# Kernel optimization log

Hardware: AMD Instinct MI355X
Metric: run time of the kernel (lower is better)

Reference implementation:

```python
import jax, jax.numpy as jnp
import numpy as np

E = 250000   # n_scanned_edges
B = 16       # batch_size
N = 50000    # n_entities (n_nodes)
R = 500      # n_relations
D_IN = 100   # input embedding dim (proj input)
D = 64       # n_dims_sm
M = 2 * E    # n_memorized_and_scanned_nodes (>= n_vi_groups + n_vj_groups)


def setup_inputs() -> dict:
    rng = np.random.default_rng(0)
    eg = rng.integers(0, B, E)
    vi = rng.integers(0, N, E)
    vj = rng.integers(0, N, E)
    order = np.lexsort((vj, vi, eg))  # sorted by (eg_idx, vi, vj) as the module assumes
    eg, vi, vj = eg[order], vi[order], vj[order]
    rel = rng.integers(0, R, E)
    # dense group ids; idx_vi is non-decreasing because edges are lexsorted by (eg,vi)
    idx_vi = np.unique(eg.astype(np.int64) * N + vi, return_inverse=True)[1]
    idx_vj = np.unique(eg.astype(np.int64) * N + vj, return_inverse=True)[1]
    n_vi = int(idx_vi.max()) + 1
    edges = np.stack([eg, vi, vj, rel, idx_vi, idx_vj, idx_vi, n_vi + idx_vj], 1).astype(np.int32)

    key = jax.random.key(0)
    ks = jax.random.split(key, 24)
    nrm = lambda k, shp, s=1.0: jax.random.normal(k, shp, jnp.float32) * s
    na = jax.random.uniform(ks[0], (B, N), jnp.float32)
    na = na / jnp.sum(na, 1, keepdims=True)  # node attention is a distribution per example
    inp = {
        "node_attention": na,
        "scanned_edges": jnp.asarray(edges),
        "hidden_uncon": nrm(ks[1], (1, N, D_IN)),
        "hidden_con": nrm(ks[2], (M, D_IN)),
        "rel_table": nrm(ks[3], (R, D_IN)),
        "query_head_emb": nrm(ks[4], (B, D_IN)),
        "query_rel_emb": nrm(ks[5], (B, D_IN)),
        "p_W": nrm(ks[6], (D_IN, D), 0.1),
        "p_b": jnp.zeros((D,), jnp.float32),
    }
    i = 7
    for g in ("g1", "g2"):
        for nm, shp in (("lW", (4 * D, D)), ("lb", (D,)), ("rW", (4 * D, D)), ("rb", (D,)), ("cW", (D, D)), ("cb", (D,))):
            inp[g + "_" + nm] = nrm(ks[i], shp, 0.05)
            i += 1
    return inp


def _g(left, right, lW, lb, rW, rb, cW, cb):
    # G layer: sum(left_dense(cat(left)) * center_dense(right_dense(cat(right))), -1)
    lx = jnp.concatenate(left, -1)
    rx = jnp.concatenate(right, -1)
    l = jax.nn.leaky_relu(lx @ lW + lb, 0.2)  # tf.nn.leaky_relu alpha=0.2
    r = jax.nn.leaky_relu(rx @ rW + rb, 0.2)
    return jnp.sum(l * (r @ cW + cb), -1)


def reference(node_attention, scanned_edges, hidden_uncon, hidden_con, rel_table,
              query_head_emb, query_rel_emb, p_W, p_b,
              g1_lW, g1_lb, g1_rW, g1_rb, g1_cW, g1_cb,
              g2_lW, g2_lb, g2_rW, g2_rb, g2_cW, g2_cb):
    Bn, Nn = node_attention.shape
    En = scanned_edges.shape[0]
    proj = lambda x: jnp.tanh(x @ p_W + p_b)

    h_con = proj(hidden_con)       # (M, D)
    h_uncon = proj(hidden_uncon)   # (1, N, D)
    qh = proj(query_head_emb)      # (B, D)
    qr = proj(query_rel_emb)

    e = scanned_edges
    eg, vi, vj = e[:, 0], e[:, 1], e[:, 2]
    idx_vi = e[:, 4]
    # node2edge gathers
    h_vi = h_con[e[:, 6]]          # (E, D)
    h_vj = h_con[e[:, 7]]
    hu_vj = h_uncon[0][vj]         # hidden_uncon batch is 1 -> idx 0
    remb = proj(rel_table[e[:, 3]])
    qhv = qh[eg]
    qrv = qr[eg]

    left = (h_vi, remb, qhv, qrv)
    logits = _g(left, (h_vj, remb, qhv, qrv), g1_lW, g1_lb, g1_rW, g1_rb, g1_cW, g1_cb)
    logits = logits + _g(left, (hu_vj, remb, qhv, qrv), g2_lW, g2_lb, g2_rW, g2_rb, g2_cW, g2_cb)

    # neighbor softmax over sorted idx_vi segments
    m = jax.ops.segment_max(logits, idx_vi, num_segments=En, indices_are_sorted=True)
    ex = jnp.exp(logits - m[idx_vi])
    den = jax.ops.segment_sum(ex, idx_vi, num_segments=En, indices_are_sorted=True)
    transition = ex / den[idx_vi]

    # flow attention: gather at (eg, vi), scatter-sum at (eg, vj)
    trans_att = node_attention[eg, vi] * transition
    new_att = jnp.zeros((Bn, Nn), node_attention.dtype).at[eg, vj].add(trans_att)
    new_att = new_att / jnp.sum(new_att, axis=1, keepdims=True)
    return new_att
```

## Files before the change

### kernel.cpp

```cpp
#include <hip/hip_runtime.h>

#define DIN 100
#define DD  64
#define NE  250000
#define NB  16
#define NN  50000
#define NR  500
#define NM  500000
#define NH  (NM + NN)

#define H_OFF    64
#define TA2_OFF  (H_OFF + NH*DD)
#define RT_OFF   (TA2_OFF + NE*DD)
#define QT_OFF   (RT_OFF + 4*NR*DD)
#define LG_OFF   (QT_OFF + 4*NB*DD)

#define PA 320
#define PB 160
#define PC 32

#define XT_STRIDE 260

__device__ __forceinline__ void fma4x4(const float4 x, const float4 w, float4 acc[4]) {
  acc[0].x += x.x*w.x; acc[0].y += x.x*w.y; acc[0].z += x.x*w.z; acc[0].w += x.x*w.w;
  acc[1].x += x.y*w.x; acc[1].y += x.y*w.y; acc[1].z += x.y*w.z; acc[1].w += x.y*w.w;
  acc[2].x += x.z*w.x; acc[2].y += x.z*w.y; acc[2].z += x.z*w.z; acc[2].w += x.z*w.w;
  acc[3].x += x.w*w.x; acc[3].y += x.w*w.y; acc[3].z += x.w*w.z; acc[3].w += x.w*w.w;
}

__device__ __forceinline__ float4 leaky4(float4 v) {
  v.x = v.x > 0.f ? v.x : 0.2f*v.x;
  v.y = v.y > 0.f ? v.y : 0.2f*v.y;
  v.z = v.z > 0.f ? v.z : 0.2f*v.z;
  v.w = v.w > 0.f ? v.w : 0.2f*v.w;
  return v;
}

__global__ void k_init(int* wsI, float* bsum) {
  if (threadIdx.x == 0) { wsI[0] = 0x7fffffff; wsI[1] = 0; }
  if (threadIdx.x < NB) bsum[threadIdx.x] = 0.f;
}

__global__ void k_limits(const int* __restrict__ edges, int* __restrict__ wsI) {
  int i = blockIdx.x * blockDim.x + threadIdx.x;
  int mn = 0x7fffffff, mx = -1;
  if (i < NE) { int v = edges[i*8 + 7]; mn = v; mx = v; }
  for (int off = 32; off > 0; off >>= 1) {
    mn = min(mn, __shfl_down(mn, off));
    mx = max(mx, __shfl_down(mx, off));
  }
  if ((threadIdx.x & 63) == 0) {
    atomicMin(&wsI[0], mn);
    atomicMax(&wsI[1], mx + 1);
  }
}

__global__ void k_tables(const float* __restrict__ rtab,
                         const float* __restrict__ qh, const float* __restrict__ qr,
                         const float* __restrict__ pW, const float* __restrict__ pb,
                         const float* __restrict__ g1_lW, const float* __restrict__ g1_lb,
                         const float* __restrict__ g1_rW, const float* __restrict__ g1_rb,
                         const float* __restrict__ g2_lW, const float* __restrict__ g2_lb,
                         const float* __restrict__ g2_rW, const float* __restrict__ g2_rb,
                         float* __restrict__ rT, float* __restrict__ qT) {
  __shared__ float xs[DIN], xs2[DIN], ps[DD], ps2[DD];
  const int d = threadIdx.x;
  const int blk = blockIdx.x;
  if (blk < NR) {
    for (int k = d; k < DIN; k += 64) xs[k] = rtab[blk*DIN + k];
    __syncthreads();
    float a = pb[d];
    for (int k = 0; k < DIN; ++k) a += xs[k] * pW[k*DD + d];
    ps[d] = tanhf(a);
    __syncthreads();
    float o1 = 0.f, o2 = 0.f, o3 = 0.f, o4 = 0.f;
    for (int k = 0; k < DD; ++k) {
      float p = ps[k];
      o1 += p * g1_lW[(DD + k)*DD + d];
      o2 += p * g1_rW[(DD + k)*DD + d];
      o3 += p * g2_lW[(DD + k)*DD + d];
      o4 += p * g2_rW[(DD + k)*DD + d];
    }
    rT[(0*NR + blk)*DD + d] = o1;
    rT[(1*NR + blk)*DD + d] = o2;
    rT[(2*NR + blk)*DD + d] = o3;
    rT[(3*NR + blk)*DD + d] = o4;
  } else {
    const int b = blk - NR;
    for (int k = d; k < DIN; k += 64) { xs[k] = qh[b*DIN + k]; xs2[k] = qr[b*DIN + k]; }
    __syncthreads();
    float a = pb[d], a2 = pb[d];
    for (int k = 0; k < DIN; ++k) { a += xs[k]*pW[k*DD + d]; a2 += xs2[k]*pW[k*DD + d]; }
    ps[d] = tanhf(a); ps2[d] = tanhf(a2);
    __syncthreads();
    float o1 = g1_lb[d], o2 = g1_rb[d], o3 = g2_lb[d], o4 = g2_rb[d];
    for (int k = 0; k < DD; ++k) {
      float p = ps[k], p2 = ps2[k];
      o1 += p * g1_lW[(2*DD + k)*DD + d] + p2 * g1_lW[(3*DD + k)*DD + d];
      o2 += p * g1_rW[(2*DD + k)*DD + d] + p2 * g1_rW[(3*DD + k)*DD + d];
      o3 += p * g2_lW[(2*DD + k)*DD + d] + p2 * g2_lW[(3*DD + k)*DD + d];
      o4 += p * g2_rW[(2*DD + k)*DD + d] + p2 * g2_rW[(3*DD + k)*DD + d];
    }
    qT[(0*NB + b)*DD + d] = o1;
    qT[(1*NB + b)*DD + d] = o2;
    qT[(2*NB + b)*DD + d] = o3;
    qT[(3*NB + b)*DD + d] = o4;
  }
}

__global__ __launch_bounds__(256, 2)
void k_proj(const float* __restrict__ hcon, const float* __restrict__ huncon,
            const float* __restrict__ pW, const float* __restrict__ pb,
            const int* __restrict__ lim, float* __restrict__ H) {
  __shared__ __align__(16) float pWs[DIN*DD];
  __shared__ __align__(16) float Xt[52][XT_STRIDE];
  const int tid = threadIdx.x;
  for (int i = tid; i < DIN*DD; i += 256) pWs[i] = pW[i];
  const int tc = tid & 7, tr = tid >> 3;
  const int c0 = tc << 3;
  const float4 pb0 = *(const float4*)&pb[c0];
  const float4 pb1 = *(const float4*)&pb[c0 + 4];
  const int nmax = lim[1];
  const int t_lo = (nmax + 255) >> 8;
  const int NT   = t_lo + ((NN + 255) >> 8);
  __syncthreads();
  for (int t = blockIdx.x; t < NT; t += gridDim.x) {
    const int row0 = (t < t_lo) ? (t << 8) : (NM + ((t - t_lo) << 8));
    const int myrow = row0 + tid;
    const float* src = nullptr;
    if (myrow < NH) src = (myrow < NM) ? &hcon[myrow*DIN] : &huncon[(myrow - NM)*DIN];
    float4 acc[2][2][4];
    #pragma unroll
    for (int a = 0; a < 2; ++a)
      #pragma unroll
      for (int b = 0; b < 2; ++b)
        #pragma unroll
        for (int i = 0; i < 4; ++i) acc[a][b][i] = make_float4(0.f,0.f,0.f,0.f);
    #pragma unroll
    for (int chunk = 0; chunk < 2; ++chunk) {
      const int kb = chunk ? 48 : 0;
      const int klen = chunk ? 52 : 48;
      __syncthreads();
      if (src) {
        for (int j = 0; j < klen; j += 4) {
          float4 v = *(const float4*)&src[kb + j];
          Xt[j+0][tid] = v.x; Xt[j+1][tid] = v.y; Xt[j+2][tid] = v.z; Xt[j+3][tid] = v.w;
        }
      }
      __syncthreads();
      for (int k = 0; k < klen; ++k) {
        float4 x0 = *(const float4*)&Xt[k][tr*8];
        float4 x1 = *(const float4*)&Xt[k][tr*8 + 4];
        float4 w0 = *(const float4*)&pWs[(kb + k)*DD + c0];
        float4 w1 = *(const float4*)&pWs[(kb + k)*DD + c0 + 4];
        fma4x4(x0, w0, acc[0][0]); fma4x4(x0, w1, acc[0][1]);
        fma4x4(x1, w0, acc[1][0]); fma4x4(x1, w1, acc[1][1]);
      }
    }
    #pragma unroll
    for (int a = 0; a < 2; ++a)
      #pragma unroll
      for (int i = 0; i < 4; ++i) {
        int row = row0 + tr*8 + a*4 + i;
        if (row < NH) {
          float4 o0, o1;
          o0.x = tanhf(acc[a][0][i].x + pb0.x);
          o0.y = tanhf(acc[a][0][i].y + pb0.y);
          o0.z = tanhf(acc[a][0][i].z + pb0.z);
          o0.w = tanhf(acc[a][0][i].w + pb0.w);
          o1.x = tanhf(acc[a][1][i].x + pb1.x);
          o1.y = tanhf(acc[a][1][i].y + pb1.y);
          o1.z = tanhf(acc[a][1][i].z + pb1.z);
          o1.w = tanhf(acc[a][1][i].w + pb1.w);
          *(float4*)&H[row*DD + c0]     = o0;
          *(float4*)&H[row*DD + c0 + 4] = o1;
        }
      }
  }
}

__global__ __launch_bounds__(256, 2)
void k_tf(const float* __restrict__ g1_lW, const float* __restrict__ g1_rW,
          const float* __restrict__ g2_lW, const float* __restrict__ g2_rW,
          const int* __restrict__ lim,
          float* __restrict__ H, float* __restrict__ TA2) {
  __shared__ __align__(16) float Ws0[DD*DD];
  __shared__ __align__(16) float Ws1[DD*DD];
  __shared__ __align__(16) float Ht[32][XT_STRIDE];
  const int tid = threadIdx.x;
  const int nvi  = lim[0];
  const int nmax = lim[1];
  int pool, pbase, pgrid;
  if (blockIdx.x < PA)           { pool = 0; pbase = blockIdx.x;           pgrid = PA; }
  else if (blockIdx.x < PA + PB) { pool = 1; pbase = blockIdx.x - PA;      pgrid = PB; }
  else                           { pool = 2; pbase = blockIdx.x - PA - PB; pgrid = PC; }
  if (pool == 0) {
    for (int i = tid; i < DD*DD; i += 256) { Ws0[i] = g1_lW[i]; Ws1[i] = g2_lW[i]; }
  } else if (pool == 1) {
    for (int i = tid; i < DD*DD; i += 256) Ws0[i] = g1_rW[i];
  } else {
    for (int i = tid; i < DD*DD; i += 256) Ws0[i] = g2_rW[i];
  }
  int t_begin, t_count, row_base;
  if (pool == 0)      { t_begin = 0;        t_count = (nvi + 255) >> 8;                 row_base = 0;  }
  else if (pool == 1) { t_begin = nvi >> 8; t_count = ((nmax + 255) >> 8) - (nvi >> 8); row_base = 0;  }
  else                { t_begin = 0;        t_count = (NN + 255) >> 8;                  row_base = NM; }
  const int tc = tid & 7, tr = tid >> 3;
  const int c0 = tc << 3;
  __syncthreads();
  for (int tt = pbase; tt < t_count; tt += pgrid) {
    const int row0 = row_base + ((t_begin + tt) << 8);
    const int myrow = row0 + tid;
    float4 a0[2][2][4], a1[2][2][4];
    #pragma unroll
    for (int a = 0; a < 2; ++a)
      #pragma unroll
      for (int b = 0; b < 2; ++b)
        #pragma unroll
        for (int i = 0; i < 4; ++i) {
          a0[a][b][i] = make_float4(0.f,0.f,0.f,0.f);
          a1[a][b][i] = make_float4(0.f,0.f,0.f,0.f);
        }
    #pragma unroll
    for (int chunk = 0; chunk < 2; ++chunk) {
      const int kb = chunk << 5;
      __syncthreads();
      if (myrow < NH) {
        const float* src = &H[myrow*DD + kb];
        #pragma unroll
        for (int j = 0; j < 32; j += 4) {
          float4 v = *(const float4*)&src[j];
          Ht[j+0][tid] = v.x; Ht[j+1][tid] = v.y; Ht[j+2][tid] = v.z; Ht[j+3][tid] = v.w;
        }
      }
      __syncthreads();
      if (pool == 0) {
        for (int k = 0; k < 32; ++k) {
          float4 x0 = *(const float4*)&Ht[k][tr*8];
          float4 x1 = *(const float4*)&Ht[k][tr*8 + 4];
          float4 w0 = *(const float4*)&Ws0[(kb + k)*DD + c0];
          float4 w1 = *(const float4*)&Ws0[(kb + k)*DD + c0 + 4];
          float4 u0 = *(const float4*)&Ws1[(kb + k)*DD + c0];
          float4 u1 = *(const float4*)&Ws1[(kb + k)*DD + c0 + 4];
          fma4x4(x0, w0, a0[0][0]); fma4x4(x0, w1, a0[0][1]);
          fma4x4(x1, w0, a0[1][0]); fma4x4(x1, w1, a0[1][1]);
          fma4x4(x0, u0, a1[0][0]); fma4x4(x0, u1, a1[0][1]);
          fma4x4(x1, u0, a1[1][0]); fma4x4(x1, u1, a1[1][1]);
        }
      } else {
        for (int k = 0; k < 32; ++k) {
          float4 x0 = *(const float4*)&Ht[k][tr*8];
          float4 x1 = *(const float4*)&Ht[k][tr*8 + 4];
          float4 w0 = *(const float4*)&Ws0[(kb + k)*DD + c0];
          float4 w1 = *(const float4*)&Ws0[(kb + k)*DD + c0 + 4];
          fma4x4(x0, w0, a0[0][0]); fma4x4(x0, w1, a0[0][1]);
          fma4x4(x1, w0, a0[1][0]); fma4x4(x1, w1, a0[1][1]);
        }
      }
    }
    #pragma unroll
    for (int a = 0; a < 2; ++a)
      #pragma unroll
      for (int i = 0; i < 4; ++i) {
        int row = row0 + tr*8 + a*4 + i;
        bool ok;
        if (pool == 0)      ok = (row < nvi);
        else if (pool == 1) ok = (row >= nvi && row < nmax);
        else                ok = (row < NH);
        if (ok) {
          *(float4*)&H[row*DD + c0]     = a0[a][0][i];
          *(float4*)&H[row*DD + c0 + 4] = a0[a][1][i];
          if (pool == 0) {
            *(float4*)&TA2[row*DD + c0]     = a1[a][0][i];
            *(float4*)&TA2[row*DD + c0 + 4] = a1[a][1][i];
          }
        }
      }
  }
}

__global__ __launch_bounds__(256, 2)
void k_edges(const int* __restrict__ edges,
             const float* __restrict__ TA, const float* __restrict__ TA2,
             const float* __restrict__ HU2,
             const float* __restrict__ rT, const float* __restrict__ qT,
             const float* __restrict__ cW1, const float* __restrict__ cb1,
             const float* __restrict__ cW2, const float* __restrict__ cb2,
             float* __restrict__ logits) {
  __shared__ __align__(16) float Wt1s[DD*68];
  __shared__ __align__(16) float Wt2s[DD*68];
  __shared__ __align__(16) float Lt[DD][68];
  __shared__ __align__(16) float Rt[DD][68];
  __shared__ __align__(16) float4 cbs4[2][16];
  __shared__ float lg[64];
  __shared__ int   se[64*8];
  const int tid = threadIdx.x;
  for (int i = tid; i < DD*DD; i += 256) {
    int k = i >> 6, d = i & 63;
    Wt1s[d*68 + k] = cW1[i];
    Wt2s[d*68 + k] = cW2[i];
  }
  if (tid < 16) {
    cbs4[0][tid] = *(const float4*)&cb1[tid*4];
    cbs4[1][tid] = *(const float4*)&cb2[tid*4];
  }
  const int e   = tid >> 2;
  const int d0  = (tid & 3) * 16;
  const int ee0 = (tid & 15) << 2;
  const int k0  = (tid >> 4) << 2;
  __syncthreads();
  const int NT = (NE + 63) / 64;
  for (int tile = blockIdx.x; tile < NT; tile += gridDim.x) {
    const int e0 = tile * 64;
    const int ecnt = min(64, NE - e0);
    for (int i = tid; i < 64*8; i += 256) se[i] = (i < ecnt*8) ? edges[e0*8 + i] : 0;
    if (tid < 64) lg[tid] = 0.f;
    __syncthreads();
    const int rel = se[e*8 + 3];
    const int eg  = se[e*8 + 0];
    const int li  = se[e*8 + 6];
    for (int g = 0; g < 2; ++g) {
      const float* Lb = g ? TA2 : TA;
      const float* Rb = g ? HU2 : TA;
      const float* rL = rT + (g ? 2*NR*DD : 0);
      const float* rR = rT + (g ? 3*NR*DD : 1*NR*DD);
      const float* qL = qT + (g ? 2*NB*DD : 0);
      const float* qR = qT + (g ? 3*NB*DD : 1*NB*DD);
      const float* Wts = g ? Wt2s : Wt1s;
      const int ri = g ? se[e*8 + 2] : se[e*8 + 7];
      float cbp = 0.f;
      #pragma unroll
      for (int di = 0; di < 4; ++di) {
        const int d = d0 + 4*di;
        float4 l = *(const float4*)&Lb[li*DD + d];
        float4 t = *(const float4*)&rL[rel*DD + d];
        float4 u = *(const float4*)&qL[eg*DD + d];
        l.x += t.x + u.x; l.y += t.y + u.y; l.z += t.z + u.z; l.w += t.w + u.w;
        l = leaky4(l);
        Lt[d+0][e] = l.x; Lt[d+1][e] = l.y; Lt[d+2][e] = l.z; Lt[d+3][e] = l.w;
        float4 c = cbs4[g][d >> 2];
        cbp += l.x*c.x + l.y*c.y + l.z*c.z + l.w*c.w;
        float4 r = *(const float4*)&Rb[ri*DD + d];
        t = *(const float4*)&rR[rel*DD + d];
        u = *(const float4*)&qR[eg*DD + d];
        r.x += t.x + u.x; r.y += t.y + u.y; r.z += t.z + u.z; r.w += t.w + u.w;
        r = leaky4(r);
        Rt[d+0][e] = r.x; Rt[d+1][e] = r.y; Rt[d+2][e] = r.z; Rt[d+3][e] = r.w;
      }
      atomicAdd(&lg[e], cbp);
      __syncthreads();
      float4 z[4] = {{0,0,0,0},{0,0,0,0},{0,0,0,0},{0,0,0,0}};
      for (int d = 0; d < DD; ++d) {
        float4 x = *(const float4*)&Lt[d][ee0];
        float4 w = *(const float4*)&Wts[d*68 + k0];
        fma4x4(x, w, z);
      }
      {
        float4 r0v = *(const float4*)&Rt[k0+0][ee0];
        float4 r1v = *(const float4*)&Rt[k0+1][ee0];
        float4 r2v = *(const float4*)&Rt[k0+2][ee0];
        float4 r3v = *(const float4*)&Rt[k0+3][ee0];
        float p0 = z[0].x*r0v.x + z[0].y*r1v.x + z[0].z*r2v.x + z[0].w*r3v.x;
        float p1 = z[1].x*r0v.y + z[1].y*r1v.y + z[1].z*r2v.y + z[1].w*r3v.y;
        float p2 = z[2].x*r0v.z + z[2].y*r1v.z + z[2].z*r2v.z + z[2].w*r3v.z;
        float p3 = z[3].x*r0v.w + z[3].y*r1v.w + z[3].z*r2v.w + z[3].w*r3v.w;
        atomicAdd(&lg[ee0+0], p0);
        atomicAdd(&lg[ee0+1], p1);
        atomicAdd(&lg[ee0+2], p2);
        atomicAdd(&lg[ee0+3], p3);
      }
      __syncthreads();
    }
    if (tid < ecnt) logits[e0 + tid] = lg[tid];
    __syncthreads();
  }
}

__global__ void k_softmax(const int* __restrict__ edges, const float* __restrict__ logits,
                          const float* __restrict__ na, float* __restrict__ out) {
  int e = blockIdx.x * blockDim.x + threadIdx.x;
  if (e >= NE) return;
  int seg = edges[e*8 + 4];
  if (e > 0 && edges[(e-1)*8 + 4] == seg) return;
  int j = e;
  float m = -1e30f;
  while (j < NE && edges[j*8 + 4] == seg) { m = fmaxf(m, logits[j]); ++j; }
  float s = 0.f;
  for (int t = e; t < j; ++t) s += expf(logits[t] - m);
  int eg = edges[e*8 + 0], vi = edges[e*8 + 1];
  float scale = na[eg*NN + vi] / s;
  for (int t = e; t < j; ++t) {
    int vj = edges[t*8 + 2];
    __hip_atomic_fetch_add(&out[eg*NN + vj], expf(logits[t] - m) * scale,
                           __ATOMIC_RELAXED, __HIP_MEMORY_SCOPE_AGENT);
  }
}

__global__ void k_rowsum(const float* __restrict__ out, float* __restrict__ bsum) {
  int b = blockIdx.y;
  float s = 0.f;
  for (int n = blockIdx.x * blockDim.x + threadIdx.x; n < NN; n += gridDim.x * blockDim.x)
    s += out[b*NN + n];
  for (int off = 32; off > 0; off >>= 1) s += __shfl_down(s, off);
  if ((threadIdx.x & 63) == 0)
    __hip_atomic_fetch_add(&bsum[b], s, __ATOMIC_RELAXED, __HIP_MEMORY_SCOPE_AGENT);
}

__global__ void k_div(float* __restrict__ out, const float* __restrict__ bsum) {
  int i = blockIdx.x * blockDim.x + threadIdx.x;
  if (i < NB*NN) out[i] /= bsum[i / NN];
}

extern "C" void kernel_launch(void* const* d_in, const int* in_sizes, int n_in,
                              void* d_out, int out_size, void* d_ws, size_t ws_size,
                              hipStream_t stream) {
  (void)in_sizes; (void)n_in; (void)out_size; (void)ws_size;
  const float* na     = (const float*)d_in[0];
  const int*   edges  = (const int*)  d_in[1];
  const float* huncon = (const float*)d_in[2];
  const float* hcon   = (const float*)d_in[3];
  const float* rtab   = (const float*)d_in[4];
  const float* qh     = (const float*)d_in[5];
  const float* qr     = (const float*)d_in[6];
  const float* pW     = (const float*)d_in[7];
  const float* pb     = (const float*)d_in[8];
  const float* g1_lW  = (const float*)d_in[9];
  const float* g1_lb  = (const float*)d_in[10];
  const float* g1_rW  = (const float*)d_in[11];
  const float* g1_rb  = (const float*)d_in[12];
  const float* g1_cW  = (const float*)d_in[13];
  const float* g1_cb  = (const float*)d_in[14];
  const float* g2_lW  = (const float*)d_in[15];
  const float* g2_lb  = (const float*)d_in[16];
  const float* g2_rW  = (const float*)d_in[17];
  const float* g2_rb  = (const float*)d_in[18];
  const float* g2_cW  = (const float*)d_in[19];
  const float* g2_cb  = (const float*)d_in[20];
  float* out  = (float*)d_out;
  float* ws   = (float*)d_ws;
  int*   wsI  = (int*)d_ws;
  float* bsum = ws + 16;
  float* H    = ws + H_OFF;
  float* TA2  = ws + TA2_OFF;
  float* rT   = ws + RT_OFF;
  float* qT   = ws + QT_OFF;
  float* lgp  = ws + LG_OFF;

  hipMemsetAsync(d_out, 0, (size_t)NB*NN*sizeof(float), stream);
  k_init<<<1, 64, 0, stream>>>(wsI, bsum);
  k_limits<<<(NE + 255)/256, 256, 0, stream>>>(edges, wsI);
  k_tables<<<NR + NB, 64, 0, stream>>>(rtab, qh, qr, pW, pb,
                                       g1_lW, g1_lb, g1_rW, g1_rb,
                                       g2_lW, g2_lb, g2_rW, g2_rb, rT, qT);
  k_proj<<<512, 256, 0, stream>>>(hcon, huncon, pW, pb, wsI, H);
  k_tf<<<PA + PB + PC, 256, 0, stream>>>(g1_lW, g1_rW, g2_lW, g2_rW, wsI, H, TA2);
  k_edges<<<512, 256, 0, stream>>>(edges, H, TA2, H + NM*DD, rT, qT,
                                   g1_cW, g1_cb, g2_cW, g2_cb, lgp);
  k_softmax<<<(NE + 255)/256, 256, 0, stream>>>(edges, lgp, na, out);
  k_rowsum<<<dim3(32, 16), 256, 0, stream>>>(out, bsum);
  k_div<<<(NB*NN + 255)/256, 256, 0, stream>>>(out, bsum);
}
```

Before: 816.8 us.

## Load GEMM rows directly from global, drop LDS transposes, shuffle-reduce edge logits

k_proj and k_tf no longer stage input rows through a transposed LDS tile. Each thread now loads float4 chunks of its 8 rows straight from global memory, and k_tf uses a shared gemm64 helper for its two passes. This removes the shared-memory footprint and the block barriers, which allows 3 blocks per CU and larger grids. k_edges remaps its threads so each partial logit is summed with a 16-lane xor-shuffle and written once, replacing four LDS atomics per thread. The trade-off is that the global loads become strided and uncoalesced, relying on the cache for reuse, and in-place H updates in k_tf now depend on a single barrier.

Result: slower. 860.4 us (+5.3%).

```diff
diff --git a/kernel.cpp b/kernel.cpp
--- a/kernel.cpp
+++ b/kernel.cpp
@@ -15,17 +15,19 @@
 #define QT_OFF   (RT_OFF + 4*NR*DD)
 #define LG_OFF   (QT_OFF + 4*NB*DD)
 
-#define PA 320
-#define PB 160
-#define PC 32
-
-#define XT_STRIDE 260
+#define PA 475
+#define PB 238
+#define PC 55
 
 __device__ __forceinline__ void fma4x4(const float4 x, const float4 w, float4 acc[4]) {
   acc[0].x += x.x*w.x; acc[0].y += x.x*w.y; acc[0].z += x.x*w.z; acc[0].w += x.x*w.w;
   acc[1].x += x.y*w.x; acc[1].y += x.y*w.y; acc[1].z += x.y*w.z; acc[1].w += x.y*w.w;
   acc[2].x += x.z*w.x; acc[2].y += x.z*w.y; acc[2].z += x.z*w.z; acc[2].w += x.z*w.w;
   acc[3].x += x.w*w.x; acc[3].y += x.w*w.y; acc[3].z += x.w*w.z; acc[3].w += x.w*w.w;
+}
+
+__device__ __forceinline__ float fc(const float4& v, int i) {
+  return ((const float*)&v)[i];
 }
 
 __device__ __forceinline__ float4 leaky4(float4 v) {
@@ -108,12 +110,11 @@
   }
 }
 
-__global__ __launch_bounds__(256, 2)
+__global__ __launch_bounds__(256, 3)
 void k_proj(const float* __restrict__ hcon, const float* __restrict__ huncon,
             const float* __restrict__ pW, const float* __restrict__ pb,
             const int* __restrict__ lim, float* __restrict__ H) {
   __shared__ __align__(16) float pWs[DIN*DD];
-  __shared__ __align__(16) float Xt[52][XT_STRIDE];
   const int tid = threadIdx.x;
   for (int i = tid; i < DIN*DD; i += 256) pWs[i] = pW[i];
   const int tc = tid & 7, tr = tid >> 3;
@@ -125,10 +126,16 @@
   const int NT   = t_lo + ((NN + 255) >> 8);
   __syncthreads();
   for (int t = blockIdx.x; t < NT; t += gridDim.x) {
-    const int row0 = (t < t_lo) ? (t << 8) : (NM + ((t - t_lo) << 8));
-    const int myrow = row0 + tid;
-    const float* src = nullptr;
-    if (myrow < NH) src = (myrow < NM) ? &hcon[myrow*DIN] : &huncon[(myrow - NM)*DIN];
+    const bool lo = (t < t_lo);
+    const int row0 = lo ? (t << 8) : (NM + ((t - t_lo) << 8));
+    const int rlim = lo ? nmax : NH;
+    const float* srcs[8];
+    #pragma unroll
+    for (int r = 0; r < 8; ++r) {
+      int row = row0 + tr*8 + r;
+      if (row >= rlim) row = rlim - 1;
+      srcs[r] = lo ? &hcon[(size_t)row*DIN] : &huncon[(size_t)(row - NM)*DIN];
+    }
     float4 acc[2][2][4];
     #pragma unroll
     for (int a = 0; a < 2; ++a)
@@ -136,25 +143,18 @@
       for (int b = 0; b < 2; ++b)
         #pragma unroll
         for (int i = 0; i < 4; ++i) acc[a][b][i] = make_float4(0.f,0.f,0.f,0.f);
-    #pragma unroll
-    for (int chunk = 0; chunk < 2; ++chunk) {
-      const int kb = chunk ? 48 : 0;
-      const int klen = chunk ? 52 : 48;
-      __syncthreads();
-      if (src) {
-        for (int j = 0; j < klen; j += 4) {
-          float4 v = *(const float4*)&src[kb + j];
-          Xt[j+0][tid] = v.x; Xt[j+1][tid] = v.y; Xt[j+2][tid] = v.z; Xt[j+3][tid] = v.w;
-        }
-      }
-      __syncthreads();
-      for (int k = 0; k < klen; ++k) {
-        float4 x0 = *(const float4*)&Xt[k][tr*8];
-        float4 x1 = *(const float4*)&Xt[k][tr*8 + 4];
-        float4 w0 = *(const float4*)&pWs[(kb + k)*DD + c0];
-        float4 w1 = *(const float4*)&pWs[(kb + k)*DD + c0 + 4];
-        fma4x4(x0, w0, acc[0][0]); fma4x4(x0, w1, acc[0][1]);
-        fma4x4(x1, w0, acc[1][0]); fma4x4(x1, w1, acc[1][1]);
+    for (int kb = 0; kb < DIN; kb += 4) {
+      float4 xv[8];
+      #pragma unroll
+      for (int r = 0; r < 8; ++r) xv[r] = *(const float4*)(srcs[r] + kb);
+      #pragma unroll
+      for (int kk = 0; kk < 4; ++kk) {
+        float4 w0 = *(const float4*)&pWs[(kb + kk)*DD + c0];
+        float4 w1 = *(const float4*)&pWs[(kb + kk)*DD + c0 + 4];
+        float4 xa = make_float4(fc(xv[0],kk), fc(xv[1],kk), fc(xv[2],kk), fc(xv[3],kk));
+        float4 xb = make_float4(fc(xv[4],kk), fc(xv[5],kk), fc(xv[6],kk), fc(xv[7],kk));
+        fma4x4(xa, w0, acc[0][0]); fma4x4(xa, w1, acc[0][1]);
+        fma4x4(xb, w0, acc[1][0]); fma4x4(xb, w1, acc[1][1]);
       }
     }
     #pragma unroll
@@ -162,7 +162,7 @@
       #pragma unroll
       for (int i = 0; i < 4; ++i) {
         int row = row0 + tr*8 + a*4 + i;
-        if (row < NH) {
+        if (row < rlim) {
           float4 o0, o1;
           o0.x = tanhf(acc[a][0][i].x + pb0.x);
           o0.y = tanhf(acc[a][0][i].y + pb0.y);
@@ -172,21 +172,44 @@
           o1.y = tanhf(acc[a][1][i].y + pb1.y);
           o1.z = tanhf(acc[a][1][i].z + pb1.z);
           o1.w = tanhf(acc[a][1][i].w + pb1.w);
-          *(float4*)&H[row*DD + c0]     = o0;
-          *(float4*)&H[row*DD + c0 + 4] = o1;
+          *(float4*)&H[(size_t)row*DD + c0]     = o0;
+          *(float4*)&H[(size_t)row*DD + c0 + 4] = o1;
         }
       }
   }
 }
 
-__global__ __launch_bounds__(256, 2)
+__device__ __forceinline__ void gemm64(const float* const* srcs, const float* __restrict__ Wss,
+                                       int c0, float4 acc[2][2][4]) {
+  #pragma unroll
+  for (int a = 0; a < 2; ++a)
+    #pragma unroll
+    for (int b = 0; b < 2; ++b)
+      #pragma unroll
+      for (int i = 0; i < 4; ++i) acc[a][b][i] = make_float4(0.f,0.f,0.f,0.f);
+  for (int kb = 0; kb < DD; kb += 4) {
+    float4 xv[8];
+    #pragma unroll
+    for (int r = 0; r < 8; ++r) xv[r] = *(const float4*)(srcs[r] + kb);
+    #pragma unroll
+    for (int kk = 0; kk < 4; ++kk) {
+      float4 w0 = *(const float4*)&Wss[(kb + kk)*DD + c0];
+      float4 w1 = *(const float4*)&Wss[(kb + kk)*DD + c0 + 4];
+      float4 xa = make_float4(fc(xv[0],kk), fc(xv[1],kk), fc(xv[2],kk), fc(xv[3],kk));
+      float4 xb = make_float4(fc(xv[4],kk), fc(xv[5],kk), fc(xv[6],kk), fc(xv[7],kk));
+      fma4x4(xa, w0, acc[0][0]); fma4x4(xa, w1, acc[0][1]);
+      fma4x4(xb, w0, acc[1][0]); fma4x4(xb, w1, acc[1][1]);
+    }
+  }
+}
+
+__global__ __launch_bounds__(256, 3)
 void k_tf(const float* __restrict__ g1_lW, const float* __restrict__ g1_rW,
           const float* __restrict__ g2_lW, const float* __restrict__ g2_rW,
           const int* __restrict__ lim,
           float* __restrict__ H, float* __restrict__ TA2) {
   __shared__ __align__(16) float Ws0[DD*DD];
   __shared__ __align__(16) float Ws1[DD*DD];
-  __shared__ __align__(16) float Ht[32][XT_STRIDE];
   const int tid = threadIdx.x;
   const int nvi  = lim[0];
   const int nmax = lim[1];
@@ -201,79 +224,46 @@
   } else {
     for (int i = tid; i < DD*DD; i += 256) Ws0[i] = g2_rW[i];
   }
-  int t_begin, t_count, row_base;
-  if (pool == 0)      { t_begin = 0;        t_count = (nvi + 255) >> 8;                 row_base = 0;  }
-  else if (pool == 1) { t_begin = nvi >> 8; t_count = ((nmax + 255) >> 8) - (nvi >> 8); row_base = 0;  }
-  else                { t_begin = 0;        t_count = (NN + 255) >> 8;                  row_base = NM; }
+  int t_begin, t_count, row_base, rlim, wlo, whi;
+  if (pool == 0)      { t_begin = 0;        t_count = (nvi + 255) >> 8;                 row_base = 0;  rlim = nmax; wlo = 0;   whi = nvi;  }
+  else if (pool == 1) { t_begin = nvi >> 8; t_count = ((nmax + 255) >> 8) - (nvi >> 8); row_base = 0;  rlim = nmax; wlo = nvi; whi = nmax; }
+  else                { t_begin = 0;        t_count = (NN + 255) >> 8;                  row_base = NM; rlim = NH;   wlo = NM;  whi = NH;   }
   const int tc = tid & 7, tr = tid >> 3;
   const int c0 = tc << 3;
   __syncthreads();
   for (int tt = pbase; tt < t_count; tt += pgrid) {
     const int row0 = row_base + ((t_begin + tt) << 8);
-    const int myrow = row0 + tid;
-    float4 a0[2][2][4], a1[2][2][4];
-    #pragma unroll
-    for (int a = 0; a < 2; ++a)
-      #pragma unroll
-      for (int b = 0; b < 2; ++b)
+    const float* srcs[8];
+    #pragma unroll
+    for (int r = 0; r < 8; ++r) {
+      int row = row0 + tr*8 + r;
+      if (row >= rlim) row = rlim - 1;
+      srcs[r] = &H[(size_t)row*DD];
+    }
+    float4 acc[2][2][4];
+    if (pool == 0) {
+      gemm64(srcs, Ws1, c0, acc);
+      #pragma unroll
+      for (int a = 0; a < 2; ++a)
         #pragma unroll
         for (int i = 0; i < 4; ++i) {
-          a0[a][b][i] = make_float4(0.f,0.f,0.f,0.f);
-          a1[a][b][i] = make_float4(0.f,0.f,0.f,0.f);
+          int row = row0 + tr*8 + a*4 + i;
+          if (row >= wlo && row < whi) {
+            *(float4*)&TA2[(size_t)row*DD + c0]     = acc[a][0][i];
+            *(float4*)&TA2[(size_t)row*DD + c0 + 4] = acc[a][1][i];
+          }
         }
-    #pragma unroll
-    for (int chunk = 0; chunk < 2; ++chunk) {
-      const int kb = chunk << 5;
-      __syncthreads();
-      if (myrow < NH) {
-        const float* src = &H[myrow*DD + kb];
-        #pragma unroll
-        for (int j = 0; j < 32; j += 4) {
-          float4 v = *(const float4*)&src[j];
-          Ht[j+0][tid] = v.x; Ht[j+1][tid] = v.y; Ht[j+2][tid] = v.z; Ht[j+3][tid] = v.w;
-        }
-      }
-      __syncthreads();
-      if (pool == 0) {
-        for (int k = 0; k < 32; ++k) {
-          float4 x0 = *(const float4*)&Ht[k][tr*8];
-          float4 x1 = *(const float4*)&Ht[k][tr*8 + 4];
-          float4 w0 = *(const float4*)&Ws0[(kb + k)*DD + c0];
-          float4 w1 = *(const float4*)&Ws0[(kb + k)*DD + c0 + 4];
-          float4 u0 = *(const float4*)&Ws1[(kb + k)*DD + c0];
-          float4 u1 = *(const float4*)&Ws1[(kb + k)*DD + c0 + 4];
-          fma4x4(x0, w0, a0[0][0]); fma4x4(x0, w1, a0[0][1]);
-          fma4x4(x1, w0, a0[1][0]); fma4x4(x1, w1, a0[1][1]);
-          fma4x4(x0, u0, a1[0][0]); fma4x4(x0, u1, a1[0][1]);
-          fma4x4(x1, u0, a1[1][0]); fma4x4(x1, u1, a1[1][1]);
-        }
-      } else {
-        for (int k = 0; k < 32; ++k) {
-          float4 x0 = *(const float4*)&Ht[k][tr*8];
-          float4 x1 = *(const float4*)&Ht[k][tr*8 + 4];
-          float4 w0 = *(const float4*)&Ws0[(kb + k)*DD + c0];
-          float4 w1 = *(const float4*)&Ws0[(kb + k)*DD + c0 + 4];
-          fma4x4(x0, w0, a0[0][0]); fma4x4(x0, w1, a0[0][1]);
-          fma4x4(x1, w0, a0[1][0]); fma4x4(x1, w1, a0[1][1]);
-        }
-      }
-    }
+    }
+    gemm64(srcs, Ws0, c0, acc);
+    __syncthreads();
     #pragma unroll
     for (int a = 0; a < 2; ++a)
       #pragma unroll
       for (int i = 0; i < 4; ++i) {
         int row = row0 + tr*8 + a*4 + i;
-        bool ok;
-        if (pool == 0)      ok = (row < nvi);
-        else if (pool == 1) ok = (row >= nvi && row < nmax);
-        else                ok = (row < NH);
-        if (ok) {
-          *(float4*)&H[row*DD + c0]     = a0[a][0][i];
-          *(float4*)&H[row*DD + c0 + 4] = a0[a][1][i];
-          if (pool == 0) {
-            *(float4*)&TA2[row*DD + c0]     = a1[a][0][i];
-            *(float4*)&TA2[row*DD + c0 + 4] = a1[a][1][i];
-          }
+        if (row >= wlo && row < whi) {
+          *(float4*)&H[(size_t)row*DD + c0]     = acc[a][0][i];
+          *(float4*)&H[(size_t)row*DD + c0 + 4] = acc[a][1][i];
         }
       }
   }
@@ -306,8 +296,8 @@
   }
   const int e   = tid >> 2;
   const int d0  = (tid & 3) * 16;
-  const int ee0 = (tid & 15) << 2;
-  const int k0  = (tid >> 4) << 2;
+  const int eq0 = (tid >> 4) << 2;
+  const int jq0 = (tid & 15) << 2;
   __syncthreads();
   const int NT = (NE + 63) / 64;
   for (int tile = blockIdx.x; tile < NT; tile += gridDim.x) {
@@ -332,7 +322,7 @@
       #pragma unroll
       for (int di = 0; di < 4; ++di) {
         const int d = d0 + 4*di;
-        float4 l = *(const float4*)&Lb[li*DD + d];
+        float4 l = *(const float4*)&Lb[(size_t)li*DD + d];
         float4 t = *(const float4*)&rL[rel*DD + d];
         float4 u = *(const float4*)&qL[eg*DD + d];
         l.x += t.x + u.x; l.y += t.y + u.y; l.z += t.z + u.z; l.w += t.w + u.w;
@@ -340,7 +330,7 @@
         Lt[d+0][e] = l.x; Lt[d+1][e] = l.y; Lt[d+2][e] = l.z; Lt[d+3][e] = l.w;
         float4 c = cbs4[g][d >> 2];
         cbp += l.x*c.x + l.y*c.y + l.z*c.z + l.w*c.w;
-        float4 r = *(const float4*)&Rb[ri*DD + d];
+        float4 r = *(const float4*)&Rb[(size_t)ri*DD + d];
         t = *(const float4*)&rR[rel*DD + d];
         u = *(const float4*)&qR[eg*DD + d];
         r.x += t.x + u.x; r.y += t.y + u.y; r.z += t.z + u.z; r.w += t.w + u.w;
@@ -351,23 +341,30 @@
       __syncthreads();
       float4 z[4] = {{0,0,0,0},{0,0,0,0},{0,0,0,0},{0,0,0,0}};
       for (int d = 0; d < DD; ++d) {
-        float4 x = *(const float4*)&Lt[d][ee0];
-        float4 w = *(const float4*)&Wts[d*68 + k0];
+        float4 x = *(const float4*)&Lt[d][eq0];
+        float4 w = *(const float4*)&Wts[d*68 + jq0];
         fma4x4(x, w, z);
       }
-      {
-        float4 r0v = *(const float4*)&Rt[k0+0][ee0];
-        float4 r1v = *(const float4*)&Rt[k0+1][ee0];
-        float4 r2v = *(const float4*)&Rt[k0+2][ee0];
-        float4 r3v = *(const float4*)&Rt[k0+3][ee0];
-        float p0 = z[0].x*r0v.x + z[0].y*r1v.x + z[0].z*r2v.x + z[0].w*r3v.x;
-        float p1 = z[1].x*r0v.y + z[1].y*r1v.y + z[1].z*r2v.y + z[1].w*r3v.y;
-        float p2 = z[2].x*r0v.z + z[2].y*r1v.z + z[2].z*r2v.z + z[2].w*r3v.z;
-        float p3 = z[3].x*r0v.w + z[3].y*r1v.w + z[3].z*r2v.w + z[3].w*r3v.w;
-        atomicAdd(&lg[ee0+0], p0);
-        atomicAdd(&lg[ee0+1], p1);
-        atomicAdd(&lg[ee0+2], p2);
-        atomicAdd(&lg[ee0+3], p3);
+      float4 rv0 = *(const float4*)&Rt[jq0+0][eq0];
+      float4 rv1 = *(const float4*)&Rt[jq0+1][eq0];
+      float4 rv2 = *(const float4*)&Rt[jq0+2][eq0];
+      float4 rv3 = *(const float4*)&Rt[jq0+3][eq0];
+      float p0 = z[0].x*rv0.x + z[0].y*rv1.x + z[0].z*rv2.x + z[0].w*rv3.x;
+      float p1 = z[1].x*rv0.y + z[1].y*rv1.y + z[1].z*rv2.y + z[1].w*rv3.y;
+      float p2 = z[2].x*rv0.z + z[2].y*rv1.z + z[2].z*rv2.z + z[2].w*rv3.z;
+      float p3 = z[3].x*rv0.w + z[3].y*rv1.w + z[3].z*rv2.w + z[3].w*rv3.w;
+      #pragma unroll
+      for (int m = 1; m < 16; m <<= 1) {
+        p0 += __shfl_xor(p0, m);
+        p1 += __shfl_xor(p1, m);
+        p2 += __shfl_xor(p2, m);
+        p3 += __shfl_xor(p3, m);
+      }
+      if ((tid & 15) == 0) {
+        lg[eq0+0] += p0;
+        lg[eq0+1] += p1;
+        lg[eq0+2] += p2;
+        lg[eq0+3] += p3;
       }
       __syncthreads();
     }
@@ -452,7 +449,7 @@
   k_tables<<<NR + NB, 64, 0, stream>>>(rtab, qh, qr, pW, pb,
                                        g1_lW, g1_lb, g1_rW, g1_rb,
                                        g2_lW, g2_lb, g2_rW, g2_rb, rT, qT);
-  k_proj<<<512, 256, 0, stream>>>(hcon, huncon, pW, pb, wsI, H);
+  k_proj<<<768, 256, 0, stream>>>(hcon, huncon, pW, pb, wsI, H);
   k_tf<<<PA + PB + PC, 256, 0, stream>>>(g1_lW, g1_rW, g2_lW, g2_rW, wsI, H, TA2);
   k_edges<<<512, 256, 0, stream>>>(edges, H, TA2, H + NM*DD, rT, qT,
                                    g1_cW, g1_cb, g2_cW, g2_cb, lgp);
```
